# Kernel optimization log

Hardware: AMD Instinct MI355X
Metric: run time of the kernel (lower is better)

The kernel has to match this reference:

```python
import jax, jax.numpy as jnp
import numpy as np

N_NODES = 50000
N_EDGES = 800000
NODE_DIM = 128
EDGE_DIM = 10
IN_DIM = 2 * NODE_DIM + EDGE_DIM
BN_EPS = 1e-5


def setup_inputs() -> dict:
    key = jax.random.key(0)
    ks = jax.random.split(key, 8)
    h = jax.random.normal(ks[0], (N_NODES, NODE_DIM), dtype=jnp.float32)
    edge_index = jax.random.randint(ks[1], (2, N_EDGES), 0, N_NODES, dtype=jnp.int64)
    edge_feat = jax.random.normal(ks[2], (N_EDGES, EDGE_DIM), dtype=jnp.float32)
    scale = 1.0 / np.sqrt(IN_DIM)
    gate_w = jax.random.normal(ks[3], (IN_DIM, NODE_DIM), dtype=jnp.float32) * scale
    gate_b = jax.random.normal(ks[4], (NODE_DIM,), dtype=jnp.float32) * scale
    cand_w = jax.random.normal(ks[5], (IN_DIM, NODE_DIM), dtype=jnp.float32) * scale
    cand_b = jax.random.normal(ks[6], (NODE_DIM,), dtype=jnp.float32) * scale
    bn_gamma = jnp.ones((NODE_DIM,), dtype=jnp.float32)
    bn_beta = jnp.zeros((NODE_DIM,), dtype=jnp.float32)
    return {"h": h, "edge_index": edge_index, "edge_feat": edge_feat,
            "gate_w": gate_w, "gate_b": gate_b, "cand_w": cand_w, "cand_b": cand_b,
            "bn_gamma": bn_gamma, "bn_beta": bn_beta}


def reference(h, edge_index, edge_feat, gate_w, gate_b, cand_w, cand_b, bn_gamma, bn_beta):
    src = edge_index[0]
    dst = edge_index[1]
    # gather endpoint features and concat with edge features: [E, 2*D + De]
    z = jnp.concatenate([h[src], h[dst], edge_feat], axis=1)
    g = jax.nn.sigmoid(z @ gate_w + gate_b)   # [E, D]
    c = jax.nn.softplus(z @ cand_w + cand_b)  # [E, D]
    m = g * c
    # scatter-add messages to source nodes (matches index_add_(0, src, m))
    agg = jax.ops.segment_sum(m, src, num_segments=h.shape[0])
    # BatchNorm1d in training mode: batch mean / biased variance over nodes
    mean = jnp.mean(agg, axis=0)
    var = jnp.var(agg, axis=0)
    agg_bn = (agg - mean) * jax.lax.rsqrt(var + BN_EPS) * bn_gamma + bn_beta
    return jax.nn.softplus(h + agg_bn)
```

## Files before the change

kernel.cpp:

```cpp
#include <hip/hip_runtime.h>
#include <math.h>

#define N_NODES 50000
#define N_EDGES 800000
#define D 128
#define DE 10
#define K_TOT 266
#define TE 64
#define ZSTRIDE 296
#define MSTRIDE 129
#define WP_ELEMS (9 * 16 * 64 * 8)
#define SCAN_BLOCKS 196

typedef __bf16 bf16x8 __attribute__((ext_vector_type(8)));
typedef __bf16 bf16x4 __attribute__((ext_vector_type(4)));
typedef __bf16 bf16x2 __attribute__((ext_vector_type(2)));
typedef float  f32x4  __attribute__((ext_vector_type(4)));

__device__ __forceinline__ float fast_sigmoid(float x) {
    float t = __builtin_amdgcn_exp2f(-1.44269504089f * x);
    return __builtin_amdgcn_rcpf(1.0f + t);
}
__device__ __forceinline__ float fast_softplus(float x) {
    float t = __builtin_amdgcn_exp2f(-1.44269504089f * fabsf(x));
    return fmaxf(x, 0.0f) + 0.69314718056f * __builtin_amdgcn_logf(1.0f + t);
}

__global__ __launch_bounds__(256) void prep(
    const float* __restrict__ h, const float* __restrict__ gw,
    const float* __restrict__ cw, __bf16* __restrict__ hb,
    __bf16* __restrict__ wp, int* __restrict__ counts)
{
    int bx = blockIdx.x, t = threadIdx.x;
    if (bx < 6250) {
        int i4 = bx * 256 + t;
        float4 v = *(const float4*)&h[(size_t)i4 * 4];
        bf16x4 o = { (__bf16)v.x, (__bf16)v.y, (__bf16)v.z, (__bf16)v.w };
        *(bf16x4*)&hb[(size_t)i4 * 4] = o;
    } else if (bx < 6538) {
        int idx = (bx - 6250) * 256 + t;
        if (idx < WP_ELEMS) {
            int j    = idx & 7;
            int lane = (idx >> 3) & 63;
            int nb   = (idx >> 9) & 15;
            int kb   = idx >> 13;
            int k    = kb * 32 + ((lane >> 4) << 3) + j;
            int col  = ((nb >> 1) << 4) + (lane & 15);
            const float* w = (nb & 1) ? cw : gw;
            float v = (k < K_TOT) ? w[k * D + col] : 0.0f;
            wp[idx] = (__bf16)v;
        }
    } else {
        int n = (bx - 6538) * 256 + t;
        if (n < N_NODES) counts[n] = 0;
    }
}

__global__ __launch_bounds__(256) void csr_hist(
    const int* __restrict__ ei, int* __restrict__ counts)
{
    int e = blockIdx.x * 256 + threadIdx.x;
    atomicAdd(&counts[ei[e]], 1);
}

__global__ __launch_bounds__(256) void scan_partials(
    const int* __restrict__ counts, int* __restrict__ bsum)
{
    __shared__ int ss[256];
    int t = threadIdx.x;
    int i = blockIdx.x * 256 + t;
    int c = (i < N_NODES) ? counts[i] : 0;
    ss[t] = c;
    __syncthreads();
    #pragma unroll
    for (int off = 1; off < 256; off <<= 1) {
        int v = (t >= off) ? ss[t - off] : 0;
        __syncthreads();
        ss[t] += v;
        __syncthreads();
    }
    if (t == 255) bsum[blockIdx.x] = ss[255];
}

__global__ __launch_bounds__(256) void scan_top(
    const int* __restrict__ bsum, int* __restrict__ bbase)
{
    __shared__ int ss[256];
    int t = threadIdx.x;
    int v = (t < SCAN_BLOCKS) ? bsum[t] : 0;
    ss[t] = v;
    __syncthreads();
    #pragma unroll
    for (int off = 1; off < 256; off <<= 1) {
        int u = (t >= off) ? ss[t - off] : 0;
        __syncthreads();
        ss[t] += u;
        __syncthreads();
    }
    if (t < SCAN_BLOCKS) bbase[t] = ss[t] - v;
}

__global__ __launch_bounds__(256) void scan_final(
    const int* __restrict__ counts, const int* __restrict__ bbase,
    int* __restrict__ cursor)
{
    __shared__ int ss[256];
    int t = threadIdx.x;
    int i = blockIdx.x * 256 + t;
    int c = (i < N_NODES) ? counts[i] : 0;
    ss[t] = c;
    __syncthreads();
    #pragma unroll
    for (int off = 1; off < 256; off <<= 1) {
        int v = (t >= off) ? ss[t - off] : 0;
        __syncthreads();
        ss[t] += v;
        __syncthreads();
    }
    if (i < N_NODES) cursor[i] = bbase[blockIdx.x] + ss[t] - c;
}

__global__ __launch_bounds__(256) void csr_scatter(
    const int* __restrict__ ei, int* __restrict__ cursor,
    int* __restrict__ eidx)
{
    int e = blockIdx.x * 256 + threadIdx.x;
    int pos = atomicAdd(&cursor[ei[e]], 1);
    eidx[pos] = e;
}

__global__ __launch_bounds__(256, 4) void edge_mfma_scatter(
    const __bf16* __restrict__ hb, const int* __restrict__ ei,
    const float* __restrict__ ef, const __bf16* __restrict__ wp,
    const float* __restrict__ gb, const float* __restrict__ cb,
    const int* __restrict__ eidx, float* __restrict__ agg)
{
    __shared__ __align__(16) unsigned char smem[TE * ZSTRIDE * 2];
    __shared__ int s_eid[TE], s_src[TE], s_dst[TE];
    __bf16* zs = (__bf16*)smem;
    float*  ms = (float*)smem;

    const int t  = threadIdx.x;
    const int e0 = blockIdx.x * TE;

    if (t < TE) {
        int eid = eidx[e0 + t];
        s_eid[t] = eid;
        s_src[t] = ei[eid];
        s_dst[t] = ei[N_EDGES + eid];
    }
    __syncthreads();

    #pragma unroll
    for (int it = 0; it < 8; ++it) {
        int lin = it * 256 + t;
        int region = lin >> 10;
        int r   = (lin >> 4) & 63;
        int seg = lin & 15;
        int node = region ? s_dst[r] : s_src[r];
        bf16x8 v = *(const bf16x8*)&hb[(size_t)node * D + seg * 8];
        *(bf16x8*)&zs[r * ZSTRIDE + region * 128 + seg * 8] = v;
    }
    if (t < TE) {
        const float* efr = &ef[(size_t)s_eid[t] * DE];
        __bf16* row = &zs[t * ZSTRIDE + 256];
        #pragma unroll
        for (int j = 0; j < 5; ++j) {
            float2 a = *(const float2*)&efr[j * 2];
            bf16x2 p = { (__bf16)a.x, (__bf16)a.y };
            *(bf16x2*)&row[j * 2] = p;
        }
        *(bf16x2*)&row[10] = (bf16x2)(__bf16)0.0f;
        *(bf16x4*)&row[12] = (bf16x4)(__bf16)0.0f;
        *(bf16x8*)&row[16] = (bf16x8)(__bf16)0.0f;
        *(bf16x8*)&row[24] = (bf16x8)(__bf16)0.0f;
    }
    __syncthreads();

    const int w     = t >> 6;
    const int l     = t & 63;
    const int quad  = l >> 4;
    const int col16 = l & 15;

    f32x4 acc[4][4];
    #pragma unroll
    for (int mt = 0; mt < 4; ++mt)
        #pragma unroll
        for (int nt = 0; nt < 4; ++nt)
            acc[mt][nt] = (f32x4)0.0f;

    const __bf16* zp  = &zs[col16 * ZSTRIDE + quad * 8];
    const __bf16* wpp = &wp[(size_t)((w * 4) * 64 + l) * 8];

    #pragma unroll
    for (int kb = 0; kb < 9; ++kb) {
        bf16x8 afr[4];
        #pragma unroll
        for (int mt = 0; mt < 4; ++mt)
            afr[mt] = *(const bf16x8*)&zp[mt * 16 * ZSTRIDE + kb * 32];
        bf16x8 bfr[4];
        #pragma unroll
        for (int nt = 0; nt < 4; ++nt)
            bfr[nt] = *(const bf16x8*)&wpp[(size_t)(kb * 16 + nt) * 512];
        #pragma unroll
        for (int mt = 0; mt < 4; ++mt)
            #pragma unroll
            for (int nt = 0; nt < 4; ++nt)
                acc[mt][nt] = __builtin_amdgcn_mfma_f32_16x16x32_bf16(
                    afr[mt], bfr[nt], acc[mt][nt], 0, 0, 0);
    }
    __syncthreads();

    const int colA = w * 32 + col16;
    const int colB = colA + 16;
    const float gbA = gb[colA], cbA = cb[colA];
    const float gbB = gb[colB], cbB = cb[colB];

    #pragma unroll
    for (int mt = 0; mt < 4; ++mt) {
        #pragma unroll
        for (int r = 0; r < 4; ++r) {
            int e = mt * 16 + quad * 4 + r;
            ms[e * MSTRIDE + colA] =
                fast_sigmoid(acc[mt][0][r] + gbA) * fast_softplus(acc[mt][1][r] + cbA);
            ms[e * MSTRIDE + colB] =
                fast_sigmoid(acc[mt][2][r] + gbB) * fast_softplus(acc[mt][3][r] + cbB);
        }
    }
    __syncthreads();

    const int half = t >> 7;
    const int c    = t & 127;
    const int rlo  = half * 32, rhi = rlo + 32;
    int   cur = s_src[rlo];
    float s   = 0.0f;
    for (int e = rlo; e < rhi; ++e) {
        int node = s_src[e];
        float v  = ms[e * MSTRIDE + c];
        if (node != cur) {
            atomicAdd(&agg[(size_t)cur * D + c], s);
            s = 0.0f; cur = node;
        }
        s += v;
    }
    atomicAdd(&agg[(size_t)cur * D + c], s);
}

__global__ __launch_bounds__(256) void col_stats(
    const float* __restrict__ agg, float* __restrict__ stats)
{
    const int t    = threadIdx.x;
    const int col  = t & 127;
    const int half = t >> 7;
    float s = 0.0f, s2 = 0.0f;
    for (int r = blockIdx.x * 2 + half; r < N_NODES; r += gridDim.x * 2) {
        float v = agg[(size_t)r * D + col];
        s += v; s2 += v * v;
    }
    atomicAdd(&stats[col], s);
    atomicAdd(&stats[128 + col], s2);
}

__global__ void finalize_stats(
    const float* __restrict__ stats, const float* __restrict__ gamma,
    const float* __restrict__ beta, float* __restrict__ scbi)
{
    int c = threadIdx.x;
    const float inv_n = 1.0f / (float)N_NODES;
    float mean = stats[c] * inv_n;
    float var  = stats[128 + c] * inv_n - mean * mean;
    var = fmaxf(var, 0.0f);
    float rstd = rsqrtf(var + 1e-5f);
    float sc = rstd * gamma[c];
    scbi[c]       = sc;
    scbi[128 + c] = beta[c] - mean * sc;
}

__global__ __launch_bounds__(256) void out_softplus(
    const float* __restrict__ h, const float* __restrict__ agg,
    const float* __restrict__ scbi, float* __restrict__ out)
{
    __shared__ float sc[128], bi[128];
    int t = threadIdx.x;
    if (t < 128) { sc[t] = scbi[t]; bi[t] = scbi[128 + t]; }
    __syncthreads();
    int idx4 = blockIdx.x * 256 + t;
    int base = idx4 * 4;
    if (base < N_NODES * D) {
        float4 hv = *(const float4*)&h[base];
        float4 av = *(const float4*)&agg[base];
        int c = base & 127;
        float4 o;
        o.x = fast_softplus(hv.x + av.x * sc[c + 0] + bi[c + 0]);
        o.y = fast_softplus(hv.y + av.y * sc[c + 1] + bi[c + 1]);
        o.z = fast_softplus(hv.z + av.z * sc[c + 2] + bi[c + 2]);
        o.w = fast_softplus(hv.w + av.w * sc[c + 3] + bi[c + 3]);
        *(float4*)&out[base] = o;
    }
}

extern "C" void kernel_launch(void* const* d_in, const int* in_sizes, int n_in,
                              void* d_out, int out_size, void* d_ws, size_t ws_size,
                              hipStream_t stream) {
    const float* h     = (const float*)d_in[0];
    const int*   ei    = (const int*)  d_in[1];
    const float* ef    = (const float*)d_in[2];
    const float* gw    = (const float*)d_in[3];
    const float* gb    = (const float*)d_in[4];
    const float* cw    = (const float*)d_in[5];
    const float* cb    = (const float*)d_in[6];
    const float* gamma = (const float*)d_in[7];
    const float* beta  = (const float*)d_in[8];
    float* out = (float*)d_out;

    float*  agg     = (float*)d_ws;
    float*  stats   = agg + (size_t)N_NODES * D;
    float*  scbi    = stats + 256;
    __bf16* wp      = (__bf16*)(scbi + 256);
    __bf16* hb      = wp + WP_ELEMS;
    int*    counts  = (int*)(hb + (size_t)N_NODES * D);
    int*    cursor  = counts + N_NODES;
    int*    bsum    = cursor + N_NODES;
    int*    bbase   = bsum + 256;
    int*    eidx    = bbase + 256;

    hipMemsetAsync(d_ws, 0, ((size_t)N_NODES * D + 512) * sizeof(float), stream);
    prep<<<6734, 256, 0, stream>>>(h, gw, cw, hb, wp, counts);
    csr_hist<<<N_EDGES / 256, 256, 0, stream>>>(ei, counts);
    scan_partials<<<SCAN_BLOCKS, 256, 0, stream>>>(counts, bsum);
    scan_top<<<1, 256, 0, stream>>>(bsum, bbase);
    scan_final<<<SCAN_BLOCKS, 256, 0, stream>>>(counts, bbase, cursor);
    csr_scatter<<<N_EDGES / 256, 256, 0, stream>>>(ei, cursor, eidx);
    edge_mfma_scatter<<<N_EDGES / TE, 256, 0, stream>>>(hb, ei, ef, wp, gb, cb, eidx, agg);
    col_stats<<<200, 256, 0, stream>>>(agg, stats);
    finalize_stats<<<1, 128, 0, stream>>>(stats, gamma, beta, scbi);
    out_softplus<<<(N_NODES * D / 4 + 255) / 256, 256, 0, stream>>>(h, agg, scbi, out);
}
```

Baseline: 415.2 us.

## Make edge kernel persistent over 8 tiles with register-resident weights; fuse launches

The edge MFMA kernel now processes eight 64-edge tiles per block and loads the full bf16 weight fragment set into registers once, instead of reloading it per tile. It also prefetches the next tile's src/dst indices into a double buffer while the current tile computes. Separately, the memset and the single-block scan_top kernel are folded into the prep and scan_final kernels to cut launch count. The cost is far higher register pressure (launch bounds drop to 2 waves-per-SIMD target) and fewer blocks, which reduces occupancy and latency hiding for the irregular gathers.

```diff
diff --git a/kernel.cpp b/kernel.cpp
--- a/kernel.cpp
+++ b/kernel.cpp
@@ -7,6 +7,8 @@
 #define DE 10
 #define K_TOT 266
 #define TE 64
+#define T_TILES 8
+#define N_TILES (N_EDGES / TE)
 #define ZSTRIDE 296
 #define MSTRIDE 129
 #define WP_ELEMS (9 * 16 * 64 * 8)
@@ -29,16 +31,20 @@
 __global__ __launch_bounds__(256) void prep(
     const float* __restrict__ h, const float* __restrict__ gw,
     const float* __restrict__ cw, __bf16* __restrict__ hb,
-    __bf16* __restrict__ wp, int* __restrict__ counts)
+    __bf16* __restrict__ wp, int* __restrict__ counts,
+    float* __restrict__ agg, float* __restrict__ stats)
 {
     int bx = blockIdx.x, t = threadIdx.x;
     if (bx < 6250) {
         int i4 = bx * 256 + t;
+        *(float4*)&agg[(size_t)i4 * 4] = make_float4(0.f, 0.f, 0.f, 0.f);
+    } else if (bx < 12500) {
+        int i4 = (bx - 6250) * 256 + t;
         float4 v = *(const float4*)&h[(size_t)i4 * 4];
         bf16x4 o = { (__bf16)v.x, (__bf16)v.y, (__bf16)v.z, (__bf16)v.w };
         *(bf16x4*)&hb[(size_t)i4 * 4] = o;
-    } else if (bx < 6538) {
-        int idx = (bx - 6250) * 256 + t;
+    } else if (bx < 12788) {
+        int idx = (bx - 12500) * 256 + t;
         if (idx < WP_ELEMS) {
             int j    = idx & 7;
             int lane = (idx >> 3) & 63;
@@ -50,9 +56,11 @@
             float v = (k < K_TOT) ? w[k * D + col] : 0.0f;
             wp[idx] = (__bf16)v;
         }
+    } else if (bx < 12837) {
+        int i4 = (bx - 12788) * 256 + t;
+        if (i4 < N_NODES / 4) *(int4*)&counts[i4 * 4] = make_int4(0, 0, 0, 0);
     } else {
-        int n = (bx - 6538) * 256 + t;
-        if (n < N_NODES) counts[n] = 0;
+        if (t < 64) *(float4*)&stats[t * 4] = make_float4(0.f, 0.f, 0.f, 0.f);
     }
 }
 
@@ -82,42 +90,29 @@
     if (t == 255) bsum[blockIdx.x] = ss[255];
 }
 
-__global__ __launch_bounds__(256) void scan_top(
-    const int* __restrict__ bsum, int* __restrict__ bbase)
-{
+__global__ __launch_bounds__(256) void scan_final(
+    const int* __restrict__ counts, const int* __restrict__ bsum,
+    int* __restrict__ cursor)
+{
+    __shared__ int sb[256];
     __shared__ int ss[256];
     int t = threadIdx.x;
-    int v = (t < SCAN_BLOCKS) ? bsum[t] : 0;
-    ss[t] = v;
-    __syncthreads();
-    #pragma unroll
-    for (int off = 1; off < 256; off <<= 1) {
-        int u = (t >= off) ? ss[t - off] : 0;
-        __syncthreads();
-        ss[t] += u;
-        __syncthreads();
-    }
-    if (t < SCAN_BLOCKS) bbase[t] = ss[t] - v;
-}
-
-__global__ __launch_bounds__(256) void scan_final(
-    const int* __restrict__ counts, const int* __restrict__ bbase,
-    int* __restrict__ cursor)
-{
-    __shared__ int ss[256];
-    int t = threadIdx.x;
+    sb[t] = (t < SCAN_BLOCKS) ? bsum[t] : 0;
     int i = blockIdx.x * 256 + t;
     int c = (i < N_NODES) ? counts[i] : 0;
     ss[t] = c;
     __syncthreads();
     #pragma unroll
     for (int off = 1; off < 256; off <<= 1) {
-        int v = (t >= off) ? ss[t - off] : 0;
+        int v  = (t >= off) ? ss[t - off] : 0;
+        int vb = (t >= off) ? sb[t - off] : 0;
         __syncthreads();
         ss[t] += v;
-        __syncthreads();
-    }
-    if (i < N_NODES) cursor[i] = bbase[blockIdx.x] + ss[t] - c;
+        sb[t] += vb;
+        __syncthreads();
+    }
+    int base = blockIdx.x ? sb[blockIdx.x - 1] : 0;
+    if (i < N_NODES) cursor[i] = base + ss[t] - c;
 }
 
 __global__ __launch_bounds__(256) void csr_scatter(
@@ -129,85 +124,43 @@
     eidx[pos] = e;
 }
 
-__global__ __launch_bounds__(256, 4) void edge_mfma_scatter(
+__global__ __launch_bounds__(256, 2) void edge_mfma_scatter(
     const __bf16* __restrict__ hb, const int* __restrict__ ei,
     const float* __restrict__ ef, const __bf16* __restrict__ wp,
     const float* __restrict__ gb, const float* __restrict__ cb,
     const int* __restrict__ eidx, float* __restrict__ agg)
 {
     __shared__ __align__(16) unsigned char smem[TE * ZSTRIDE * 2];
-    __shared__ int s_eid[TE], s_src[TE], s_dst[TE];
+    __shared__ int s_eid[T_TILES * TE];
+    __shared__ int s_src[2][TE], s_dst[2][TE];
     __bf16* zs = (__bf16*)smem;
     float*  ms = (float*)smem;
 
-    const int t  = threadIdx.x;
-    const int e0 = blockIdx.x * TE;
-
-    if (t < TE) {
-        int eid = eidx[e0 + t];
-        s_eid[t] = eid;
-        s_src[t] = ei[eid];
-        s_dst[t] = ei[N_EDGES + eid];
-    }
-    __syncthreads();
-
-    #pragma unroll
-    for (int it = 0; it < 8; ++it) {
-        int lin = it * 256 + t;
-        int region = lin >> 10;
-        int r   = (lin >> 4) & 63;
-        int seg = lin & 15;
-        int node = region ? s_dst[r] : s_src[r];
-        bf16x8 v = *(const bf16x8*)&hb[(size_t)node * D + seg * 8];
-        *(bf16x8*)&zs[r * ZSTRIDE + region * 128 + seg * 8] = v;
-    }
-    if (t < TE) {
-        const float* efr = &ef[(size_t)s_eid[t] * DE];
-        __bf16* row = &zs[t * ZSTRIDE + 256];
-        #pragma unroll
-        for (int j = 0; j < 5; ++j) {
-            float2 a = *(const float2*)&efr[j * 2];
-            bf16x2 p = { (__bf16)a.x, (__bf16)a.y };
-            *(bf16x2*)&row[j * 2] = p;
-        }
-        *(bf16x2*)&row[10] = (bf16x2)(__bf16)0.0f;
-        *(bf16x4*)&row[12] = (bf16x4)(__bf16)0.0f;
-        *(bf16x8*)&row[16] = (bf16x8)(__bf16)0.0f;
-        *(bf16x8*)&row[24] = (bf16x8)(__bf16)0.0f;
-    }
-    __syncthreads();
-
+    const int t     = threadIdx.x;
     const int w     = t >> 6;
     const int l     = t & 63;
     const int quad  = l >> 4;
     const int col16 = l & 15;
-
-    f32x4 acc[4][4];
-    #pragma unroll
-    for (int mt = 0; mt < 4; ++mt)
-        #pragma unroll
-        for (int nt = 0; nt < 4; ++nt)
-            acc[mt][nt] = (f32x4)0.0f;
-
-    const __bf16* zp  = &zs[col16 * ZSTRIDE + quad * 8];
-    const __bf16* wpp = &wp[(size_t)((w * 4) * 64 + l) * 8];
-
-    #pragma unroll
-    for (int kb = 0; kb < 9; ++kb) {
-        bf16x8 afr[4];
-        #pragma unroll
-        for (int mt = 0; mt < 4; ++mt)
-            afr[mt] = *(const bf16x8*)&zp[mt * 16 * ZSTRIDE + kb * 32];
-        bf16x8 bfr[4];
-        #pragma unroll
-        for (int nt = 0; nt < 4; ++nt)
-            bfr[nt] = *(const bf16x8*)&wpp[(size_t)(kb * 16 + nt) * 512];
-        #pragma unroll
-        for (int mt = 0; mt < 4; ++mt)
+    const int tile0  = blockIdx.x * T_TILES;
+    const int ntiles = min(T_TILES, N_TILES - tile0);
+
+    bf16x8 bfr[9][4];
+    {
+        const __bf16* wpp = &wp[(size_t)((w * 4) * 64 + l) * 8];
+        #pragma unroll
+        for (int kb = 0; kb < 9; ++kb)
             #pragma unroll
             for (int nt = 0; nt < 4; ++nt)
-                acc[mt][nt] = __builtin_amdgcn_mfma_f32_16x16x32_bf16(
-                    afr[mt], bfr[nt], acc[mt][nt], 0, 0, 0);
+                bfr[kb][nt] = *(const bf16x8*)&wpp[(size_t)(kb * 16 + nt) * 512];
+    }
+
+    for (int i = t; i < ntiles * TE; i += 256)
+        s_eid[i] = eidx[tile0 * TE + i];
+    __syncthreads();
+    if (t < TE) {
+        int eid = s_eid[t];
+        s_src[0][t] = ei[eid];
+        s_dst[0][t] = ei[N_EDGES + eid];
     }
     __syncthreads();
 
@@ -216,34 +169,96 @@
     const float gbA = gb[colA], cbA = cb[colA];
     const float gbB = gb[colB], cbB = cb[colB];
 
-    #pragma unroll
-    for (int mt = 0; mt < 4; ++mt) {
-        #pragma unroll
-        for (int r = 0; r < 4; ++r) {
-            int e = mt * 16 + quad * 4 + r;
-            ms[e * MSTRIDE + colA] =
-                fast_sigmoid(acc[mt][0][r] + gbA) * fast_softplus(acc[mt][1][r] + cbA);
-            ms[e * MSTRIDE + colB] =
-                fast_sigmoid(acc[mt][2][r] + gbB) * fast_softplus(acc[mt][3][r] + cbB);
-        }
-    }
-    __syncthreads();
-
-    const int half = t >> 7;
-    const int c    = t & 127;
-    const int rlo  = half * 32, rhi = rlo + 32;
-    int   cur = s_src[rlo];
-    float s   = 0.0f;
-    for (int e = rlo; e < rhi; ++e) {
-        int node = s_src[e];
-        float v  = ms[e * MSTRIDE + c];
-        if (node != cur) {
+    for (int tile = 0; tile < ntiles; ++tile) {
+        const int buf = tile & 1;
+
+        #pragma unroll
+        for (int it = 0; it < 8; ++it) {
+            int lin = it * 256 + t;
+            int region = lin >> 10;
+            int r   = (lin >> 4) & 63;
+            int seg = lin & 15;
+            int node = region ? s_dst[buf][r] : s_src[buf][r];
+            bf16x8 v = *(const bf16x8*)&hb[(size_t)node * D + seg * 8];
+            *(bf16x8*)&zs[r * ZSTRIDE + region * 128 + seg * 8] = v;
+        }
+        if (t < TE) {
+            const float* efr = &ef[(size_t)s_eid[tile * TE + t] * DE];
+            __bf16* row = &zs[t * ZSTRIDE + 256];
+            #pragma unroll
+            for (int j = 0; j < 5; ++j) {
+                float2 a = *(const float2*)&efr[j * 2];
+                bf16x2 p = { (__bf16)a.x, (__bf16)a.y };
+                *(bf16x2*)&row[j * 2] = p;
+            }
+            *(bf16x2*)&row[10] = (bf16x2)(__bf16)0.0f;
+            *(bf16x4*)&row[12] = (bf16x4)(__bf16)0.0f;
+            *(bf16x8*)&row[16] = (bf16x8)(__bf16)0.0f;
+            *(bf16x8*)&row[24] = (bf16x8)(__bf16)0.0f;
+        }
+        __syncthreads();
+
+        if (tile + 1 < ntiles && t < TE) {
+            int eid = s_eid[(tile + 1) * TE + t];
+            s_src[buf ^ 1][t] = ei[eid];
+            s_dst[buf ^ 1][t] = ei[N_EDGES + eid];
+        }
+
+        f32x4 acc[4][4];
+        #pragma unroll
+        for (int mt = 0; mt < 4; ++mt)
+            #pragma unroll
+            for (int nt = 0; nt < 4; ++nt)
+                acc[mt][nt] = (f32x4)0.0f;
+
+        const __bf16* zp = &zs[col16 * ZSTRIDE + quad * 8];
+        #pragma unroll
+        for (int kb = 0; kb < 9; ++kb) {
+            bf16x8 afr[4];
+            #pragma unroll
+            for (int mt = 0; mt < 4; ++mt)
+                afr[mt] = *(const bf16x8*)&zp[mt * 16 * ZSTRIDE + kb * 32];
+            #pragma unroll
+            for (int mt = 0; mt < 4; ++mt)
+                #pragma unroll
+                for (int nt = 0; nt < 4; ++nt)
+                    acc[mt][nt] = __builtin_amdgcn_mfma_f32_16x16x32_bf16(
+                        afr[mt], bfr[kb][nt], acc[mt][nt], 0, 0, 0);
+        }
+        __syncthreads();
+
+        #pragma unroll
+        for (int mt = 0; mt < 4; ++mt) {
+            #pragma unroll
+            for (int r = 0; r < 4; ++r) {
+                int e = mt * 16 + quad * 4 + r;
+                ms[e * MSTRIDE + colA] =
+                    fast_sigmoid(acc[mt][0][r] + gbA) * fast_softplus(acc[mt][1][r] + cbA);
+                ms[e * MSTRIDE + colB] =
+                    fast_sigmoid(acc[mt][2][r] + gbB) * fast_softplus(acc[mt][3][r] + cbB);
+            }
+        }
+        __syncthreads();
+
+        {
+            const int half = t >> 7;
+            const int c    = t & 127;
+            const int rlo  = half * 32, rhi = rlo + 32;
+            int   cur = s_src[buf][rlo];
+            float s   = 0.0f;
+            for (int e = rlo; e < rhi; ++e) {
+                int node = s_src[buf][e];
+                float v  = ms[e * MSTRIDE + c];
+                if (node != cur) {
+                    atomicAdd(&agg[(size_t)cur * D + c], s);
+                    s = 0.0f; cur = node;
+                }
+                s += v;
+            }
             atomicAdd(&agg[(size_t)cur * D + c], s);
-            s = 0.0f; cur = node;
-        }
-        s += v;
-    }
-    atomicAdd(&agg[(size_t)cur * D + c], s);
+        }
+        __syncthreads();
+    }
 }
 
 __global__ __launch_bounds__(256) void col_stats(
@@ -321,17 +336,15 @@
     int*    counts  = (int*)(hb + (size_t)N_NODES * D);
     int*    cursor  = counts + N_NODES;
     int*    bsum    = cursor + N_NODES;
-    int*    bbase   = bsum + 256;
-    int*    eidx    = bbase + 256;
-
-    hipMemsetAsync(d_ws, 0, ((size_t)N_NODES * D + 512) * sizeof(float), stream);
-    prep<<<6734, 256, 0, stream>>>(h, gw, cw, hb, wp, counts);
+    int*    eidx    = bsum + 256;
+
+    prep<<<12838, 256, 0, stream>>>(h, gw, cw, hb, wp, counts, agg, stats);
     csr_hist<<<N_EDGES / 256, 256, 0, stream>>>(ei, counts);
     scan_partials<<<SCAN_BLOCKS, 256, 0, stream>>>(counts, bsum);
-    scan_top<<<1, 256, 0, stream>>>(bsum, bbase);
-    scan_final<<<SCAN_BLOCKS, 256, 0, stream>>>(counts, bbase, cursor);
+    scan_final<<<SCAN_BLOCKS, 256, 0, stream>>>(counts, bsum, cursor);
     csr_scatter<<<N_EDGES / 256, 256, 0, stream>>>(ei, cursor, eidx);
-    edge_mfma_scatter<<<N_EDGES / TE, 256, 0, stream>>>(hb, ei, ef, wp, gb, cb, eidx, agg);
+    edge_mfma_scatter<<<(N_TILES + T_TILES - 1) / T_TILES, 256, 0, stream>>>(
+        hb, ei, ef, wp, gb, cb, eidx, agg);
     col_stats<<<200, 256, 0, stream>>>(agg, stats);
     finalize_stats<<<1, 128, 0, stream>>>(stats, gamma, beta, scbi);
     out_softplus<<<(N_NODES * D / 4 + 255) / 256, 256, 0, stream>>>(h, agg, scbi, out);
```

New measurement: 568.2 us. 36.8% more time.

## Split edge GEMM K into two staged halves, shrink LDS, merge small kernels

Applied to the files above, without the earlier changes.

The edge kernel now stages the source-node slice and multiplies it, then reuses the same smaller LDS buffer for the destination slice plus edge features. This cuts shared memory per block so the launch bound can rise to 6 blocks per CU. Messages are staged in LDS as bf16 instead of fp32 before the segmented scatter-add, which loses some precision. Separately, the histogram is folded into the prep kernel, the top-level scan is recomputed redundantly inside scan_final, and finalize_stats is merged into out_softplus, which removes three launches.

```diff
diff --git a/kernel.cpp b/kernel.cpp
--- a/kernel.cpp
+++ b/kernel.cpp
@@ -7,8 +7,11 @@
 #define DE 10
 #define K_TOT 266
 #define TE 64
-#define ZSTRIDE 296
-#define MSTRIDE 129
+#define N_TILES (N_EDGES / TE)
+#define ZS1 136
+#define ZS2 168
+#define MS 130
+#define SMEM_BYTES (TE * ZS2 * 2)
 #define WP_ELEMS (9 * 16 * 64 * 8)
 #define SCAN_BLOCKS 196
 
@@ -28,8 +31,9 @@
 
 __global__ __launch_bounds__(256) void prep(
     const float* __restrict__ h, const float* __restrict__ gw,
-    const float* __restrict__ cw, __bf16* __restrict__ hb,
-    __bf16* __restrict__ wp, int* __restrict__ counts)
+    const float* __restrict__ cw, const int* __restrict__ ei,
+    __bf16* __restrict__ hb, __bf16* __restrict__ wp,
+    int* __restrict__ counts)
 {
     int bx = blockIdx.x, t = threadIdx.x;
     if (bx < 6250) {
@@ -51,16 +55,9 @@
             wp[idx] = (__bf16)v;
         }
     } else {
-        int n = (bx - 6538) * 256 + t;
-        if (n < N_NODES) counts[n] = 0;
-    }
-}
-
-__global__ __launch_bounds__(256) void csr_hist(
-    const int* __restrict__ ei, int* __restrict__ counts)
-{
-    int e = blockIdx.x * 256 + threadIdx.x;
-    atomicAdd(&counts[ei[e]], 1);
+        int e = (bx - 6538) * 256 + t;
+        atomicAdd(&counts[ei[e]], 1);
+    }
 }
 
 __global__ __launch_bounds__(256) void scan_partials(
@@ -82,42 +79,29 @@
     if (t == 255) bsum[blockIdx.x] = ss[255];
 }
 
-__global__ __launch_bounds__(256) void scan_top(
-    const int* __restrict__ bsum, int* __restrict__ bbase)
-{
+__global__ __launch_bounds__(256) void scan_final(
+    const int* __restrict__ counts, const int* __restrict__ bsum,
+    int* __restrict__ cursor)
+{
+    __shared__ int sb[256];
     __shared__ int ss[256];
     int t = threadIdx.x;
-    int v = (t < SCAN_BLOCKS) ? bsum[t] : 0;
-    ss[t] = v;
-    __syncthreads();
-    #pragma unroll
-    for (int off = 1; off < 256; off <<= 1) {
-        int u = (t >= off) ? ss[t - off] : 0;
-        __syncthreads();
-        ss[t] += u;
-        __syncthreads();
-    }
-    if (t < SCAN_BLOCKS) bbase[t] = ss[t] - v;
-}
-
-__global__ __launch_bounds__(256) void scan_final(
-    const int* __restrict__ counts, const int* __restrict__ bbase,
-    int* __restrict__ cursor)
-{
-    __shared__ int ss[256];
-    int t = threadIdx.x;
+    sb[t] = (t < SCAN_BLOCKS) ? bsum[t] : 0;
     int i = blockIdx.x * 256 + t;
     int c = (i < N_NODES) ? counts[i] : 0;
     ss[t] = c;
     __syncthreads();
     #pragma unroll
     for (int off = 1; off < 256; off <<= 1) {
-        int v = (t >= off) ? ss[t - off] : 0;
+        int v  = (t >= off) ? ss[t - off] : 0;
+        int vb = (t >= off) ? sb[t - off] : 0;
         __syncthreads();
         ss[t] += v;
+        sb[t] += vb;
         __syncthreads();
     }
-    if (i < N_NODES) cursor[i] = bbase[blockIdx.x] + ss[t] - c;
+    int base = blockIdx.x ? sb[blockIdx.x - 1] : 0;
+    if (i < N_NODES) cursor[i] = base + ss[t] - c;
 }
 
 __global__ __launch_bounds__(256) void csr_scatter(
@@ -129,19 +113,23 @@
     eidx[pos] = e;
 }
 
-__global__ __launch_bounds__(256, 4) void edge_mfma_scatter(
+__global__ __launch_bounds__(256, 6) void edge_mfma_scatter(
     const __bf16* __restrict__ hb, const int* __restrict__ ei,
     const float* __restrict__ ef, const __bf16* __restrict__ wp,
     const float* __restrict__ gb, const float* __restrict__ cb,
     const int* __restrict__ eidx, float* __restrict__ agg)
 {
-    __shared__ __align__(16) unsigned char smem[TE * ZSTRIDE * 2];
+    __shared__ __align__(16) unsigned char smem[SMEM_BYTES];
     __shared__ int s_eid[TE], s_src[TE], s_dst[TE];
-    __bf16* zs = (__bf16*)smem;
-    float*  ms = (float*)smem;
-
-    const int t  = threadIdx.x;
-    const int e0 = blockIdx.x * TE;
+    __bf16* zs  = (__bf16*)smem;
+    __bf16* msb = (__bf16*)smem;
+
+    const int t     = threadIdx.x;
+    const int w     = t >> 6;
+    const int l     = t & 63;
+    const int quad  = l >> 4;
+    const int col16 = l & 15;
+    const int e0    = blockIdx.x * TE;
 
     if (t < TE) {
         int eid = eidx[e0 + t];
@@ -151,19 +139,58 @@
     }
     __syncthreads();
 
-    #pragma unroll
-    for (int it = 0; it < 8; ++it) {
+    f32x4 acc[4][4];
+    #pragma unroll
+    for (int mt = 0; mt < 4; ++mt)
+        #pragma unroll
+        for (int nt = 0; nt < 4; ++nt)
+            acc[mt][nt] = (f32x4)0.0f;
+
+    const __bf16* wpp = &wp[(size_t)((w * 4) * 64 + l) * 8];
+
+    #pragma unroll
+    for (int it = 0; it < 4; ++it) {
         int lin = it * 256 + t;
-        int region = lin >> 10;
-        int r   = (lin >> 4) & 63;
+        int r   = lin >> 4;
         int seg = lin & 15;
-        int node = region ? s_dst[r] : s_src[r];
-        bf16x8 v = *(const bf16x8*)&hb[(size_t)node * D + seg * 8];
-        *(bf16x8*)&zs[r * ZSTRIDE + region * 128 + seg * 8] = v;
+        bf16x8 v = *(const bf16x8*)&hb[(size_t)s_src[r] * D + seg * 8];
+        *(bf16x8*)&zs[r * ZS1 + seg * 8] = v;
+    }
+    __syncthreads();
+
+    {
+        const __bf16* zp = &zs[col16 * ZS1 + quad * 8];
+        #pragma unroll
+        for (int kb = 0; kb < 4; ++kb) {
+            bf16x8 afr[4];
+            #pragma unroll
+            for (int mt = 0; mt < 4; ++mt)
+                afr[mt] = *(const bf16x8*)&zp[mt * 16 * ZS1 + kb * 32];
+            bf16x8 bfr[4];
+            #pragma unroll
+            for (int nt = 0; nt < 4; ++nt)
+                bfr[nt] = *(const bf16x8*)&wpp[(size_t)(kb * 16 + nt) * 512];
+            #pragma unroll
+            for (int mt = 0; mt < 4; ++mt)
+                #pragma unroll
+                for (int nt = 0; nt < 4; ++nt)
+                    acc[mt][nt] = __builtin_amdgcn_mfma_f32_16x16x32_bf16(
+                        afr[mt], bfr[nt], acc[mt][nt], 0, 0, 0);
+        }
+    }
+    __syncthreads();
+
+    #pragma unroll
+    for (int it = 0; it < 4; ++it) {
+        int lin = it * 256 + t;
+        int r   = lin >> 4;
+        int seg = lin & 15;
+        bf16x8 v = *(const bf16x8*)&hb[(size_t)s_dst[r] * D + seg * 8];
+        *(bf16x8*)&zs[r * ZS2 + seg * 8] = v;
     }
     if (t < TE) {
         const float* efr = &ef[(size_t)s_eid[t] * DE];
-        __bf16* row = &zs[t * ZSTRIDE + 256];
+        __bf16* row = &zs[t * ZS2 + 128];
         #pragma unroll
         for (int j = 0; j < 5; ++j) {
             float2 a = *(const float2*)&efr[j * 2];
@@ -177,37 +204,25 @@
     }
     __syncthreads();
 
-    const int w     = t >> 6;
-    const int l     = t & 63;
-    const int quad  = l >> 4;
-    const int col16 = l & 15;
-
-    f32x4 acc[4][4];
-    #pragma unroll
-    for (int mt = 0; mt < 4; ++mt)
-        #pragma unroll
-        for (int nt = 0; nt < 4; ++nt)
-            acc[mt][nt] = (f32x4)0.0f;
-
-    const __bf16* zp  = &zs[col16 * ZSTRIDE + quad * 8];
-    const __bf16* wpp = &wp[(size_t)((w * 4) * 64 + l) * 8];
-
-    #pragma unroll
-    for (int kb = 0; kb < 9; ++kb) {
-        bf16x8 afr[4];
-        #pragma unroll
-        for (int mt = 0; mt < 4; ++mt)
-            afr[mt] = *(const bf16x8*)&zp[mt * 16 * ZSTRIDE + kb * 32];
-        bf16x8 bfr[4];
-        #pragma unroll
-        for (int nt = 0; nt < 4; ++nt)
-            bfr[nt] = *(const bf16x8*)&wpp[(size_t)(kb * 16 + nt) * 512];
-        #pragma unroll
-        for (int mt = 0; mt < 4; ++mt)
+    {
+        const __bf16* zp = &zs[col16 * ZS2 + quad * 8];
+        #pragma unroll
+        for (int kb = 0; kb < 5; ++kb) {
+            bf16x8 afr[4];
+            #pragma unroll
+            for (int mt = 0; mt < 4; ++mt)
+                afr[mt] = *(const bf16x8*)&zp[mt * 16 * ZS2 + kb * 32];
+            bf16x8 bfr[4];
             #pragma unroll
             for (int nt = 0; nt < 4; ++nt)
-                acc[mt][nt] = __builtin_amdgcn_mfma_f32_16x16x32_bf16(
-                    afr[mt], bfr[nt], acc[mt][nt], 0, 0, 0);
+                bfr[nt] = *(const bf16x8*)&wpp[(size_t)((kb + 4) * 16 + nt) * 512];
+            #pragma unroll
+            for (int mt = 0; mt < 4; ++mt)
+                #pragma unroll
+                for (int nt = 0; nt < 4; ++nt)
+                    acc[mt][nt] = __builtin_amdgcn_mfma_f32_16x16x32_bf16(
+                        afr[mt], bfr[nt], acc[mt][nt], 0, 0, 0);
+        }
     }
     __syncthreads();
 
@@ -221,29 +236,31 @@
         #pragma unroll
         for (int r = 0; r < 4; ++r) {
             int e = mt * 16 + quad * 4 + r;
-            ms[e * MSTRIDE + colA] =
-                fast_sigmoid(acc[mt][0][r] + gbA) * fast_softplus(acc[mt][1][r] + cbA);
-            ms[e * MSTRIDE + colB] =
-                fast_sigmoid(acc[mt][2][r] + gbB) * fast_softplus(acc[mt][3][r] + cbB);
-        }
-    }
-    __syncthreads();
-
-    const int half = t >> 7;
-    const int c    = t & 127;
-    const int rlo  = half * 32, rhi = rlo + 32;
-    int   cur = s_src[rlo];
-    float s   = 0.0f;
-    for (int e = rlo; e < rhi; ++e) {
-        int node = s_src[e];
-        float v  = ms[e * MSTRIDE + c];
-        if (node != cur) {
-            atomicAdd(&agg[(size_t)cur * D + c], s);
-            s = 0.0f; cur = node;
-        }
-        s += v;
-    }
-    atomicAdd(&agg[(size_t)cur * D + c], s);
+            float m0 = fast_sigmoid(acc[mt][0][r] + gbA) * fast_softplus(acc[mt][1][r] + cbA);
+            float m1 = fast_sigmoid(acc[mt][2][r] + gbB) * fast_softplus(acc[mt][3][r] + cbB);
+            msb[e * MS + colA] = (__bf16)m0;
+            msb[e * MS + colB] = (__bf16)m1;
+        }
+    }
+    __syncthreads();
+
+    {
+        const int half = t >> 7;
+        const int c    = t & 127;
+        const int rlo  = half * 32, rhi = rlo + 32;
+        int   cur = s_src[rlo];
+        float s   = 0.0f;
+        for (int e = rlo; e < rhi; ++e) {
+            int node = s_src[e];
+            float v  = (float)msb[e * MS + c];
+            if (node != cur) {
+                atomicAdd(&agg[(size_t)cur * D + c], s);
+                s = 0.0f; cur = node;
+            }
+            s += v;
+        }
+        atomicAdd(&agg[(size_t)cur * D + c], s);
+    }
 }
 
 __global__ __launch_bounds__(256) void col_stats(
@@ -261,28 +278,23 @@
     atomicAdd(&stats[128 + col], s2);
 }
 
-__global__ void finalize_stats(
-    const float* __restrict__ stats, const float* __restrict__ gamma,
-    const float* __restrict__ beta, float* __restrict__ scbi)
-{
-    int c = threadIdx.x;
-    const float inv_n = 1.0f / (float)N_NODES;
-    float mean = stats[c] * inv_n;
-    float var  = stats[128 + c] * inv_n - mean * mean;
-    var = fmaxf(var, 0.0f);
-    float rstd = rsqrtf(var + 1e-5f);
-    float sc = rstd * gamma[c];
-    scbi[c]       = sc;
-    scbi[128 + c] = beta[c] - mean * sc;
-}
-
 __global__ __launch_bounds__(256) void out_softplus(
     const float* __restrict__ h, const float* __restrict__ agg,
-    const float* __restrict__ scbi, float* __restrict__ out)
+    const float* __restrict__ stats, const float* __restrict__ gamma,
+    const float* __restrict__ beta, float* __restrict__ out)
 {
     __shared__ float sc[128], bi[128];
     int t = threadIdx.x;
-    if (t < 128) { sc[t] = scbi[t]; bi[t] = scbi[128 + t]; }
+    if (t < 128) {
+        const float inv_n = 1.0f / (float)N_NODES;
+        float mean = stats[t] * inv_n;
+        float var  = stats[128 + t] * inv_n - mean * mean;
+        var = fmaxf(var, 0.0f);
+        float rstd = rsqrtf(var + 1e-5f);
+        float s = rstd * gamma[t];
+        sc[t] = s;
+        bi[t] = beta[t] - mean * s;
+    }
     __syncthreads();
     int idx4 = blockIdx.x * 256 + t;
     int base = idx4 * 4;
@@ -315,24 +327,22 @@
 
     float*  agg     = (float*)d_ws;
     float*  stats   = agg + (size_t)N_NODES * D;
-    float*  scbi    = stats + 256;
-    __bf16* wp      = (__bf16*)(scbi + 256);
-    __bf16* hb      = wp + WP_ELEMS;
-    int*    counts  = (int*)(hb + (size_t)N_NODES * D);
+    int*    counts  = (int*)(stats + 256);
     int*    cursor  = counts + N_NODES;
     int*    bsum    = cursor + N_NODES;
-    int*    bbase   = bsum + 256;
-    int*    eidx    = bbase + 256;
-
-    hipMemsetAsync(d_ws, 0, ((size_t)N_NODES * D + 512) * sizeof(float), stream);
-    prep<<<6734, 256, 0, stream>>>(h, gw, cw, hb, wp, counts);
-    csr_hist<<<N_EDGES / 256, 256, 0, stream>>>(ei, counts);
+    __bf16* wp      = (__bf16*)(bsum + 256);
+    __bf16* hb      = wp + WP_ELEMS;
+    int*    eidx    = (int*)(hb + (size_t)N_NODES * D);
+
+    const size_t zero_bytes = ((size_t)N_NODES * D + 256) * sizeof(float)
+                            + (size_t)N_NODES * sizeof(int);
+    hipMemsetAsync(d_ws, 0, zero_bytes, stream);
+    prep<<<9663, 256, 0, stream>>>(h, gw, cw, ei, hb, wp, counts);
     scan_partials<<<SCAN_BLOCKS, 256, 0, stream>>>(counts, bsum);
-    scan_top<<<1, 256, 0, stream>>>(bsum, bbase);
-    scan_final<<<SCAN_BLOCKS, 256, 0, stream>>>(counts, bbase, cursor);
+    scan_final<<<SCAN_BLOCKS, 256, 0, stream>>>(counts, bsum, cursor);
     csr_scatter<<<N_EDGES / 256, 256, 0, stream>>>(ei, cursor, eidx);
-    edge_mfma_scatter<<<N_EDGES / TE, 256, 0, stream>>>(hb, ei, ef, wp, gb, cb, eidx, agg);
+    edge_mfma_scatter<<<N_TILES, 256, 0, stream>>>(hb, ei, ef, wp, gb, cb, eidx, agg);
     col_stats<<<200, 256, 0, stream>>>(agg, stats);
-    finalize_stats<<<1, 128, 0, stream>>>(stats, gamma, beta, scbi);
-    out_softplus<<<(N_NODES * D / 4 + 255) / 256, 256, 0, stream>>>(h, agg, scbi, out);
-}
+    out_softplus<<<(N_NODES * D / 4 + 255) / 256, 256, 0, stream>>>(
+        h, agg, stats, gamma, beta, out);
+}
```

New measurement: 1.171 ms. 2.82x slower.
